# Performance work log

Hardware: AMD Instinct MI355X
Metric: run time of the kernel (lower is better)

The kernel has to match this reference:

```python
import jax, jax.numpy as jnp
import numpy as np

J, I, N = 10, 1152, 16
BATCH = 256
SPARSE_THRESHOLD = 0.1
SPARSIFY = True
EPS = 1e-8


def squash(s):
    # squash along last (pose) dim: (|s|^2/(1+|s|^2)) * s/|s|
    sq = jnp.sum(s * s, axis=-1, keepdims=True)
    return (sq / (1.0 + sq)) * s / jnp.sqrt(sq + EPS)


def setup_inputs() -> dict:
    key = jax.random.key(0)
    k1, _ = jax.random.split(key)
    u_hat = jax.random.normal(k1, (BATCH, J, I, N), dtype=jnp.float32)
    bias = jnp.ones((J, N), dtype=jnp.float32) * 0.1  # b_routing.data.fill_(0.1)
    return {"u_hat": u_hat, "bias": bias, "iters": 3}


def reference(u_hat, bias, iters):
    b, j, i, n = u_hat.shape
    b_vec = jnp.zeros((b, j, i), dtype=u_hat.dtype)
    delete = None
    v = None
    for index in range(iters):
        # softmax over output capsules j (softmax_dim=1)
        c = jax.nn.softmax(b_vec, axis=1)                      # [b,j,i]
        s = jnp.einsum('bji,bjin->bjn', c, u_hat) + bias       # [b,j,n]
        v = squash(s)                                          # [b,j,n]
        if index < iters - 1:
            # agreement update: u_hat . v over pose dim
            b_vec = b_vec + jnp.einsum('bjin,bjn->bji', u_hat, v)
            if index == iters - 2 and SPARSIFY:
                avg_b_j = jnp.sum(b_vec, axis=2) / i           # [b,j]
                # threshold = log(thr) + logsumexp_j(avg_b_j)
                a = jnp.max(avg_b_j, axis=1)
                lse = a + jnp.log(jnp.sum(jnp.exp(avg_b_j - a[:, None]), axis=1))
                threshold = jnp.log(SPARSE_THRESHOLD) + lse    # [b]
                delete = avg_b_j < threshold[:, None]          # [b,j] bool
                b_vec = jnp.where(delete[:, :, None], -jnp.inf, b_vec)
        elif SPARSIFY and iters > 1:
            v = jnp.where(delete[:, :, None], 0.0, v)
    return v
```

## Files before the change

kernel.cpp:

```cpp
#include <hip/hip_runtime.h>
#include <hip/hip_fp16.h>
#include <math.h>

#define B_ 256
#define J_ 10
#define I_ 1152
#define N_ 16
#define TPB 512
#define STEPS0 18
#define STEPSH 9
#define JSTR (I_ * N_)
#define PSTR0 (64 * N_)
#define HJ (I_ * 16)
#define HB_BATCH (5 * HJ)
#define HSTEP0 (64 * 16)
#define HSTEPH (128 * 16)

struct alignas(16) H8 {
  __half2 a, b, c, d;
};

__device__ __forceinline__ float4 ld4(const float* p) {
  return *(const float4*)p;
}

__device__ __forceinline__ float squash16(float s) {
  float sq = s * s;
  sq += __shfl_xor(sq, 1);
  sq += __shfl_xor(sq, 2);
  sq += __shfl_xor(sq, 4);
  sq += __shfl_xor(sq, 8);
  return (sq / (1.f + sq)) * s * rsqrtf(sq + 1e-8f);
}

__device__ __forceinline__ void load5(const float* __restrict__ b0, int p,
                                      float4* t) {
#pragma unroll
  for (int jj = 0; jj < 5; ++jj)
    t[jj] = ld4(b0 + (size_t)jj * 2 * JSTR + (size_t)p * PSTR0);
}

__device__ __forceinline__ void body_sum(const float4* t, float4* acc) {
#pragma unroll
  for (int jj = 0; jj < 5; ++jj) {
    acc[jj].x += t[jj].x;
    acc[jj].y += t[jj].y;
    acc[jj].z += t[jj].z;
    acc[jj].w += t[jj].w;
  }
}

template <bool STORE>
__device__ __forceinline__ void storeh(__half2* __restrict__ sb, int p,
                                       const float4* t, bool act) {
  if (!STORE) return;
#pragma unroll
  for (int jj = 0; jj < 5; ++jj) {
    const float4 m = t[jj];
    float4 o;
    o.x = __shfl_xor(m.x, 4);
    o.y = __shfl_xor(m.y, 4);
    o.z = __shfl_xor(m.z, 4);
    o.w = __shfl_xor(m.w, 4);
    if (act) {
      H8 v;
      v.a = __floats2half2_rn(m.x, o.x);
      v.b = __floats2half2_rn(m.y, o.y);
      v.c = __floats2half2_rn(m.z, o.z);
      v.d = __floats2half2_rn(m.w, o.w);
      *(H8*)(sb + (size_t)jj * HJ + (size_t)p * HSTEP0) = v;
    }
  }
}

template <bool STORE>
__device__ __forceinline__ void run_pass0(const float* __restrict__ b0,
                                          __half2* __restrict__ sb, bool act,
                                          float4* acc) {
  float4 tA[5], tB[5];
#pragma unroll
  for (int jj = 0; jj < 5; ++jj) acc[jj] = make_float4(0.f, 0.f, 0.f, 0.f);
  load5(b0, 0, tA);
#pragma unroll 1
  for (int p = 0; p < STEPS0 - 2; p += 2) {
    load5(b0, p + 1, tB);
    storeh<STORE>(sb, p, tA, act);
    body_sum(tA, acc);
    load5(b0, p + 2, tA);
    storeh<STORE>(sb, p + 1, tB, act);
    body_sum(tB, acc);
  }
  load5(b0, STEPS0 - 1, tB);
  storeh<STORE>(sb, STEPS0 - 2, tA, act);
  body_sum(tA, acc);
  storeh<STORE>(sb, STEPS0 - 1, tB, act);
  body_sum(tB, acc);
}

__device__ __forceinline__ void load5h(const __half2* __restrict__ hbT, int p,
                                       H8* t) {
#pragma unroll
  for (int k = 0; k < 5; ++k)
    t[k] = *(const H8*)(hbT + (size_t)k * HJ + (size_t)p * HSTEPH);
}

__device__ __forceinline__ void body_h(const H8* t,
                                       const float* __restrict__ wshp, int q,
                                       unsigned dm, float4* acc) {
  float d[J_];
#pragma unroll
  for (int k = 0; k < 5; ++k) {
    const float2 f0 = __half22float2(t[k].a);
    const float2 f1 = __half22float2(t[k].b);
    const float2 f2 = __half22float2(t[k].c);
    const float2 f3 = __half22float2(t[k].d);
    const float4 wE = ld4(&wshp[(2 * k) * N_ + q * 4]);
    const float4 wO = ld4(&wshp[(2 * k + 1) * N_ + q * 4]);
    d[2 * k] = f0.x * wE.x + f1.x * wE.y + f2.x * wE.z + f3.x * wE.w;
    d[2 * k + 1] = f0.y * wO.x + f1.y * wO.y + f2.y * wO.z + f3.y * wO.w;
  }
  float se = 0.f;
#pragma unroll
  for (int j = 0; j < J_; ++j) {
    float dj = d[j];
    dj += __shfl_xor(dj, 1);
    dj += __shfl_xor(dj, 2);
    const float e = ((dm >> j) & 1u) ? 0.f : __expf(dj);
    d[j] = e;
    se += e;
  }
  const float inv = 1.f / se;
#pragma unroll
  for (int k = 0; k < 5; ++k) {
    const float2 f0 = __half22float2(t[k].a);
    const float2 f1 = __half22float2(t[k].b);
    const float2 f2 = __half22float2(t[k].c);
    const float2 f3 = __half22float2(t[k].d);
    const float cE = d[2 * k] * inv;
    const float cO = d[2 * k + 1] * inv;
    acc[2 * k].x = fmaf(cE, f0.x, acc[2 * k].x);
    acc[2 * k].y = fmaf(cE, f1.x, acc[2 * k].y);
    acc[2 * k].z = fmaf(cE, f2.x, acc[2 * k].z);
    acc[2 * k].w = fmaf(cE, f3.x, acc[2 * k].w);
    acc[2 * k + 1].x = fmaf(cO, f0.y, acc[2 * k + 1].x);
    acc[2 * k + 1].y = fmaf(cO, f1.y, acc[2 * k + 1].y);
    acc[2 * k + 1].z = fmaf(cO, f2.y, acc[2 * k + 1].z);
    acc[2 * k + 1].w = fmaf(cO, f3.y, acc[2 * k + 1].w);
  }
}

__device__ __forceinline__ void fp16_pass(const __half2* __restrict__ hbT,
                                          const float* __restrict__ wshp,
                                          int q, unsigned dm, float4* acc) {
#pragma unroll
  for (int j = 0; j < J_; ++j) acc[j] = make_float4(0.f, 0.f, 0.f, 0.f);
  H8 tA[5], tB[5];
  load5h(hbT, 0, tA);
#pragma unroll 1
  for (int p = 0; p < STEPSH - 1; p += 2) {
    load5h(hbT, p + 1, tB);
    body_h(tA, wshp, q, dm, acc);
    load5h(hbT, p + 2, tA);
    body_h(tB, wshp, q, dm, acc);
  }
  body_h(tA, wshp, q, dm, acc);
}

__device__ __forceinline__ void body_w5(const float4* t, const float4* wq,
                                        const float* mvj, float4* acc) {
  float e[5];
  float se = 0.f;
#pragma unroll
  for (int jj = 0; jj < 5; ++jj) {
    float d = t[jj].x * wq[jj].x + t[jj].y * wq[jj].y + t[jj].z * wq[jj].z +
              t[jj].w * wq[jj].w;
    d += __shfl_xor(d, 1);
    d += __shfl_xor(d, 2);
    e[jj] = __expf(d + mvj[jj]);
    se += e[jj];
  }
  se += __shfl_xor(se, 4);
  const float inv = 1.f / se;
#pragma unroll
  for (int jj = 0; jj < 5; ++jj) {
    const float c = e[jj] * inv;
    acc[jj].x = fmaf(c, t[jj].x, acc[jj].x);
    acc[jj].y = fmaf(c, t[jj].y, acc[jj].y);
    acc[jj].z = fmaf(c, t[jj].z, acc[jj].z);
    acc[jj].w = fmaf(c, t[jj].w, acc[jj].w);
  }
}

__device__ __forceinline__ void run_passw_f(const float* __restrict__ b0,
                                            const float4* wq, const float* mvj,
                                            float4* acc) {
  float4 tA[5], tB[5];
#pragma unroll
  for (int jj = 0; jj < 5; ++jj) acc[jj] = make_float4(0.f, 0.f, 0.f, 0.f);
  load5(b0, 0, tA);
#pragma unroll 1
  for (int p = 0; p < STEPS0 - 2; p += 2) {
    load5(b0, p + 1, tB);
    body_w5(tA, wq, mvj, acc);
    load5(b0, p + 2, tA);
    body_w5(tB, wq, mvj, acc);
  }
  load5(b0, STEPS0 - 1, tB);
  body_w5(tA, wq, mvj, acc);
  body_w5(tB, wq, mvj, acc);
}

__device__ __forceinline__ void block_reduce5(const float4* acc,
                                              float* __restrict__ red, int wv,
                                              int lane, int jh, int q) {
#pragma unroll
  for (int jj = 0; jj < 5; ++jj) {
    float4 a = acc[jj];
#pragma unroll
    for (int off = 8; off < 64; off <<= 1) {
      a.x += __shfl_xor(a.x, off);
      a.y += __shfl_xor(a.y, off);
      a.z += __shfl_xor(a.z, off);
      a.w += __shfl_xor(a.w, off);
    }
    if (lane < 8) {
      float* dst = &red[(((wv << 1) + jh) * 5 + jj) * 16 + q * 4];
      dst[0] = a.x;
      dst[1] = a.y;
      dst[2] = a.z;
      dst[3] = a.w;
    }
  }
  __syncthreads();
}

__device__ __forceinline__ float sum8p0(const float* __restrict__ red, int j,
                                        int n) {
  const int jh = j & 1;
  const int jj = j >> 1;
  float s = 0.f;
#pragma unroll
  for (int w = 0; w < 8; ++w) s += red[(((w << 1) + jh) * 5 + jj) * 16 + n];
  return s;
}

__device__ __forceinline__ void reduce10(const float4* acc,
                                         float* __restrict__ red, int wv,
                                         int lane, int q) {
#pragma unroll
  for (int j = 0; j < J_; ++j) {
    float4 a = acc[j];
#pragma unroll
    for (int off = 4; off < 64; off <<= 1) {
      a.x += __shfl_xor(a.x, off);
      a.y += __shfl_xor(a.y, off);
      a.z += __shfl_xor(a.z, off);
      a.w += __shfl_xor(a.w, off);
    }
    if (lane < 4) {
      float* dst = &red[(wv * J_ + j) * 16 + q * 4];
      dst[0] = a.x;
      dst[1] = a.y;
      dst[2] = a.z;
      dst[3] = a.w;
    }
  }
  __syncthreads();
}

__device__ __forceinline__ float sum8h(const float* __restrict__ red, int j,
                                       int n) {
  float s = 0.f;
#pragma unroll
  for (int w = 0; w < 8; ++w) s += red[(w * J_ + j) * 16 + n];
  return s;
}

template <int USE_FP16>
__global__ __launch_bounds__(TPB) void routing_one(
    const float* __restrict__ u, const float* __restrict__ bias,
    __half2* __restrict__ hb, float* __restrict__ out) {
  const int tid = threadIdx.x;
  const int lane = tid & 63;
  const int wv = tid >> 6;
  const int q = lane & 3;
  const int jh = (lane >> 2) & 1;
  const int rc = lane >> 3;
  const int b = blockIdx.x;
  const int row0 = wv * 8 + rc;
  const int rowh = tid >> 2;

  __shared__ float red[1280];
  __shared__ float wsh[J_ * N_];
  __shared__ float v0sh[J_ * N_];
  __shared__ float S0sh[J_ * N_];
  __shared__ float avg[J_];
  __shared__ float thr_s;

  const float* b0 = u + (size_t)b * J_ * JSTR + (size_t)jh * JSTR +
                    (size_t)row0 * N_ + q * 4;
  __half2* sb = hb + (size_t)b * HB_BATCH + (size_t)row0 * 16 + q * 4;
  const __half2* hbT = hb + (size_t)b * HB_BATCH + (size_t)rowh * 16 + q * 4;

  {
    float4 a5[5];
    run_pass0<USE_FP16 != 0>(b0, sb, jh == 0, a5);
    block_reduce5(a5, red, wv, lane, jh, q);
  }
  if (tid < J_ * N_) {
    const int j = tid >> 4, n = tid & 15;
    const float S0 = sum8p0(red, j, n);
    S0sh[tid] = S0;
    const float v0 = squash16(S0 * (1.f / (float)J_) + bias[j * N_ + n]);
    v0sh[tid] = v0;
    wsh[tid] = v0;
  }
  __syncthreads();

  if (USE_FP16) {
    {
      float4 a10[J_];
      fp16_pass(hbT, wsh, q, 0u, a10);
      reduce10(a10, red, wv, lane, q);
    }
    if (tid < J_ * N_) {
      const int j = tid >> 4, n = tid & 15;
      const float s1 = sum8h(red, j, n) + bias[j * N_ + n];
      const float v1 = squash16(s1);
      const float w2 = v0sh[tid] + v1;
      float pa = S0sh[tid] * w2;
      pa += __shfl_xor(pa, 1);
      pa += __shfl_xor(pa, 2);
      pa += __shfl_xor(pa, 4);
      pa += __shfl_xor(pa, 8);
      if (n == 0) avg[j] = pa * (1.f / (float)I_);
      wsh[tid] = w2;
    }
    __syncthreads();
    if (tid == 0) {
      float a = avg[0];
      for (int jj = 1; jj < J_; ++jj) a = fmaxf(a, avg[jj]);
      float se = 0.f;
      for (int jj = 0; jj < J_; ++jj) se += expf(avg[jj] - a);
      thr_s = logf(0.1f) + a + logf(se);
    }
    __syncthreads();
    unsigned dm = 0u;
#pragma unroll
    for (int j = 0; j < J_; ++j)
      if (avg[j] < thr_s) dm |= (1u << j);

    {
      float4 a10[J_];
      fp16_pass(hbT, wsh, q, dm, a10);
      reduce10(a10, red, wv, lane, q);
    }
    if (tid < J_ * N_) {
      const int j = tid >> 4, n = tid & 15;
      const float s2 = sum8h(red, j, n) + bias[j * N_ + n];
      const float v2 = squash16(s2);
      const bool del = avg[j] < thr_s;
      out[(b * J_ + j) * N_ + n] = del ? 0.f : v2;
    }
  } else {
    float4 wq[5];
    float mvj[5];
#pragma unroll
    for (int jj = 0; jj < 5; ++jj) {
      wq[jj] = ld4(&wsh[(2 * jj + jh) * N_ + q * 4]);
      mvj[jj] = 0.f;
    }
    {
      float4 a5[5];
      run_passw_f(b0, wq, mvj, a5);
      block_reduce5(a5, red, wv, lane, jh, q);
    }
    if (tid < J_ * N_) {
      const int j = tid >> 4, n = tid & 15;
      const float s1 = sum8p0(red, j, n) + bias[j * N_ + n];
      const float v1 = squash16(s1);
      const float w2 = v0sh[tid] + v1;
      wsh[tid] = w2;
      float pa = S0sh[tid] * w2;
      pa += __shfl_xor(pa, 1);
      pa += __shfl_xor(pa, 2);
      pa += __shfl_xor(pa, 4);
      pa += __shfl_xor(pa, 8);
      if (n == 0) avg[j] = pa * (1.f / (float)I_);
    }
    __syncthreads();
    if (tid == 0) {
      float a = avg[0];
      for (int jj = 1; jj < J_; ++jj) a = fmaxf(a, avg[jj]);
      float se = 0.f;
      for (int jj = 0; jj < J_; ++jj) se += expf(avg[jj] - a);
      thr_s = logf(0.1f) + a + logf(se);
    }
    __syncthreads();
#pragma unroll
    for (int jj = 0; jj < 5; ++jj) {
      const int j = 2 * jj + jh;
      wq[jj] = ld4(&wsh[j * N_ + q * 4]);
      mvj[jj] = (avg[j] < thr_s) ? -1e30f : 0.f;
    }
    {
      float4 a5[5];
      run_passw_f(b0, wq, mvj, a5);
      block_reduce5(a5, red, wv, lane, jh, q);
    }
    if (tid < J_ * N_) {
      const int j = tid >> 4, n = tid & 15;
      const float s2 = sum8p0(red, j, n) + bias[j * N_ + n];
      const float v2 = squash16(s2);
      const bool del = avg[j] < thr_s;
      out[(b * J_ + j) * N_ + n] = del ? 0.f : v2;
    }
  }
}

extern "C" void kernel_launch(void* const* d_in, const int* in_sizes, int n_in,
                              void* d_out, int out_size, void* d_ws,
                              size_t ws_size, hipStream_t stream) {
  const float* u = (const float*)d_in[0];
  const float* bias = (const float*)d_in[1];
  float* out = (float*)d_out;
  __half2* hb = (__half2*)d_ws;
  const size_t need = (size_t)B_ * HB_BATCH * sizeof(__half2);
  if (ws_size >= need) {
    routing_one<1><<<B_, TPB, 0, stream>>>(u, bias, hb, out);
  } else {
    routing_one<0><<<B_, TPB, 0, stream>>>(u, bias, hb, out);
  }
}
```

Baseline: 80.49 us.

## Keep first third of fp16 u_hat copy in LDS, rest in global workspace

The fp16 copy of u_hat written in pass 0 is now split: the first 384 rows per batch go into a 120 KB shared-memory buffer and the remaining 768 rows stay in the global workspace. Both later fp16 routing passes read the LDS part first, then stream the global part with the existing double-buffered loads. This cuts global/L2 write and read traffic for the staged copy. The cost is heavy LDS use that limits the kernel to one 512-thread block per CU, and the LDS reads are not software-pipelined.

```diff
diff --git a/kernel.cpp b/kernel.cpp
--- a/kernel.cpp
+++ b/kernel.cpp
@@ -8,11 +8,15 @@
 #define N_ 16
 #define TPB 512
 #define STEPS0 18
-#define STEPSH 9
+#define LSTEPS0 6
+#define LROWS 384
+#define GROWS 768
+#define LSTEPSH 3
+#define GSTEPSH 6
 #define JSTR (I_ * N_)
 #define PSTR0 (64 * N_)
-#define HJ (I_ * 16)
-#define HB_BATCH (5 * HJ)
+#define GPLANE (GROWS * 16)
+#define GBATCH (5 * GPLANE)
 #define HSTEP0 (64 * 16)
 #define HSTEPH (128 * 16)
 
@@ -51,7 +55,8 @@
 }
 
 template <bool STORE>
-__device__ __forceinline__ void storeh(__half2* __restrict__ sb, int p,
+__device__ __forceinline__ void storeh(__half2* __restrict__ sb,
+                                       H8* __restrict__ lbp, int p,
                                        const float4* t, bool act) {
   if (!STORE) return;
 #pragma unroll
@@ -68,14 +73,18 @@
       v.b = __floats2half2_rn(m.y, o.y);
       v.c = __floats2half2_rn(m.z, o.z);
       v.d = __floats2half2_rn(m.w, o.w);
-      *(H8*)(sb + (size_t)jj * HJ + (size_t)p * HSTEP0) = v;
+      if (p < LSTEPS0)
+        lbp[jj * (LROWS * 4) + p * 256] = v;
+      else
+        *(H8*)(sb + (size_t)jj * GPLANE + (size_t)(p - LSTEPS0) * HSTEP0) = v;
     }
   }
 }
 
 template <bool STORE>
 __device__ __forceinline__ void run_pass0(const float* __restrict__ b0,
-                                          __half2* __restrict__ sb, bool act,
+                                          __half2* __restrict__ sb,
+                                          H8* __restrict__ lbp, bool act,
                                           float4* acc) {
   float4 tA[5], tB[5];
 #pragma unroll
@@ -84,24 +93,24 @@
 #pragma unroll 1
   for (int p = 0; p < STEPS0 - 2; p += 2) {
     load5(b0, p + 1, tB);
-    storeh<STORE>(sb, p, tA, act);
+    storeh<STORE>(sb, lbp, p, tA, act);
     body_sum(tA, acc);
     load5(b0, p + 2, tA);
-    storeh<STORE>(sb, p + 1, tB, act);
+    storeh<STORE>(sb, lbp, p + 1, tB, act);
     body_sum(tB, acc);
   }
   load5(b0, STEPS0 - 1, tB);
-  storeh<STORE>(sb, STEPS0 - 2, tA, act);
+  storeh<STORE>(sb, lbp, STEPS0 - 2, tA, act);
   body_sum(tA, acc);
-  storeh<STORE>(sb, STEPS0 - 1, tB, act);
+  storeh<STORE>(sb, lbp, STEPS0 - 1, tB, act);
   body_sum(tB, acc);
 }
 
-__device__ __forceinline__ void load5h(const __half2* __restrict__ hbT, int p,
+__device__ __forceinline__ void load5g(const __half2* __restrict__ hbg, int p,
                                        H8* t) {
 #pragma unroll
   for (int k = 0; k < 5; ++k)
-    t[k] = *(const H8*)(hbT + (size_t)k * HJ + (size_t)p * HSTEPH);
+    t[k] = *(const H8*)(hbg + (size_t)k * GPLANE + (size_t)p * HSTEPH);
 }
 
 __device__ __forceinline__ void body_h(const H8* t,
@@ -149,21 +158,31 @@
   }
 }
 
-__device__ __forceinline__ void fp16_pass(const __half2* __restrict__ hbT,
+__device__ __forceinline__ void fp16_pass(const __half2* __restrict__ hbg,
+                                          const H8* __restrict__ lbr,
                                           const float* __restrict__ wshp,
                                           int q, unsigned dm, float4* acc) {
 #pragma unroll
   for (int j = 0; j < J_; ++j) acc[j] = make_float4(0.f, 0.f, 0.f, 0.f);
   H8 tA[5], tB[5];
-  load5h(hbT, 0, tA);
+  load5g(hbg, 0, tA);
 #pragma unroll 1
-  for (int p = 0; p < STEPSH - 1; p += 2) {
-    load5h(hbT, p + 1, tB);
+  for (int pl = 0; pl < LSTEPSH; ++pl) {
+    H8 tL[5];
+#pragma unroll
+    for (int k = 0; k < 5; ++k) tL[k] = lbr[k * (LROWS * 4) + pl * 512];
+    body_h(tL, wshp, q, dm, acc);
+  }
+#pragma unroll 1
+  for (int p = 0; p < GSTEPSH - 2; p += 2) {
+    load5g(hbg, p + 1, tB);
     body_h(tA, wshp, q, dm, acc);
-    load5h(hbT, p + 2, tA);
+    load5g(hbg, p + 2, tA);
     body_h(tB, wshp, q, dm, acc);
   }
+  load5g(hbg, GSTEPSH - 1, tB);
   body_h(tA, wshp, q, dm, acc);
+  body_h(tB, wshp, q, dm, acc);
 }
 
 __device__ __forceinline__ void body_w5(const float4* t, const float4* wq,
@@ -290,6 +309,7 @@
   const int row0 = wv * 8 + rc;
   const int rowh = tid >> 2;
 
+  __shared__ H8 lbuf[5 * LROWS * 4];
   __shared__ float red[1280];
   __shared__ float wsh[J_ * N_];
   __shared__ float v0sh[J_ * N_];
@@ -299,12 +319,14 @@
 
   const float* b0 = u + (size_t)b * J_ * JSTR + (size_t)jh * JSTR +
                     (size_t)row0 * N_ + q * 4;
-  __half2* sb = hb + (size_t)b * HB_BATCH + (size_t)row0 * 16 + q * 4;
-  const __half2* hbT = hb + (size_t)b * HB_BATCH + (size_t)rowh * 16 + q * 4;
+  __half2* sb = hb + (size_t)b * GBATCH + (size_t)row0 * 16 + q * 4;
+  const __half2* hbg = hb + (size_t)b * GBATCH + (size_t)rowh * 16 + q * 4;
+  H8* lbp = lbuf + row0 * 4 + q;
+  const H8* lbr = lbuf + rowh * 4 + q;
 
   {
     float4 a5[5];
-    run_pass0<USE_FP16 != 0>(b0, sb, jh == 0, a5);
+    run_pass0<USE_FP16 != 0>(b0, sb, lbp, jh == 0, a5);
     block_reduce5(a5, red, wv, lane, jh, q);
   }
   if (tid < J_ * N_) {
@@ -320,7 +342,7 @@
   if (USE_FP16) {
     {
       float4 a10[J_];
-      fp16_pass(hbT, wsh, q, 0u, a10);
+      fp16_pass(hbg, lbr, wsh, q, 0u, a10);
       reduce10(a10, red, wv, lane, q);
     }
     if (tid < J_ * N_) {
@@ -352,7 +374,7 @@
 
     {
       float4 a10[J_];
-      fp16_pass(hbT, wsh, q, dm, a10);
+      fp16_pass(hbg, lbr, wsh, q, dm, a10);
       reduce10(a10, red, wv, lane, q);
     }
     if (tid < J_ * N_) {
@@ -425,7 +447,7 @@
   const float* bias = (const float*)d_in[1];
   float* out = (float*)d_out;
   __half2* hb = (__half2*)d_ws;
-  const size_t need = (size_t)B_ * HB_BATCH * sizeof(__half2);
+  const size_t need = (size_t)B_ * GBATCH * sizeof(__half2);
   if (ws_size >= need) {
     routing_one<1><<<B_, TPB, 0, stream>>>(u, bias, hb, out);
   } else {
```

New measurement: 69.52 us. 13.6% less time.
